# Kernel tuning notes

Hardware: AMD Instinct MI355X
Metric: run time of the kernel (lower is better)

Reference implementation:

```python
import jax, jax.numpy as jnp
import numpy as np

DIM = 768
NUM_HEADS = 8
HEAD_DIM = DIM // NUM_HEADS
SCALE = HEAD_DIM ** -0.5


def setup_inputs() -> dict:
    key = jax.random.key(0)
    k1, k2, k3, k4 = jax.random.split(key, 4)
    B, C, H, W = 8, DIM, 32, 32
    x = jax.random.normal(k1, (B, C, H, W), dtype=jnp.float32)
    # torch Linear stores weight as (out, in); y = x @ W.T + b
    w_qkv = jax.random.normal(k2, (3 * DIM, DIM), dtype=jnp.float32) * (DIM ** -0.5)
    w_proj = jax.random.normal(k3, (DIM, DIM), dtype=jnp.float32) * (DIM ** -0.5)
    b_proj = jax.random.normal(k4, (DIM,), dtype=jnp.float32) * 0.02
    return {"x": x, "w_qkv": w_qkv, "w_proj": w_proj, "b_proj": b_proj}


def reference(x, w_qkv, w_proj, b_proj):
    B, C, H, W = x.shape
    N = H * W
    nh, hd = NUM_HEADS, HEAD_DIM
    # (B, C, H, W) -> (B, N, C)
    tokens = x.reshape(B, C, N).transpose(0, 2, 1)
    qkv = tokens @ w_qkv.T  # (B, N, 3C), no bias (qkv_bias=False)
    qkv = qkv.reshape(B, N, 3, nh, hd).transpose(2, 0, 3, 1, 4)  # (3, B, nh, N, hd)
    q, k, v = qkv[0], qkv[1], qkv[2]
    attn = jnp.einsum('bhnd,bhmd->bhnm', q, k) * SCALE
    attn = jax.nn.softmax(attn, axis=-1)  # attn_drop=0.0 (eval)
    out = jnp.einsum('bhnm,bhmd->bhnd', attn, v)  # (B, nh, N, hd)
    out = out.transpose(0, 2, 1, 3).reshape(B, N, C)
    out = out @ w_proj.T + b_proj  # proj_drop=0.0
    return out.transpose(0, 2, 1).reshape(B, C, H, W)
```

## Files before the change

### kernel.cpp

```cpp
#include <hip/hip_runtime.h>

typedef short s16x8 __attribute__((ext_vector_type(8)));
typedef short s16x4 __attribute__((ext_vector_type(4)));
typedef float f32x4 __attribute__((ext_vector_type(4)));
typedef int   i32x4 __attribute__((ext_vector_type(4)));
typedef unsigned u32x2 __attribute__((ext_vector_type(2)));

#define SCALE_F 0.10206207261596577f
#define KLOG2E  0.14724444f
#define DEFER_THR 11.5415603f

__device__ __forceinline__ unsigned short f2bf(float f) {
  unsigned u = __builtin_bit_cast(unsigned, f);
  u += 0x7fffu + ((u >> 16) & 1u);
  return (unsigned short)(u >> 16);
}
__device__ __forceinline__ unsigned cvt_pk_bf16(float a, float b) {
  unsigned r;
  asm("v_cvt_pk_bf16_f32 %0, %1, %2" : "=v"(r) : "v"(a), "v"(b));
  return r;
}
__device__ __forceinline__ float exp2_fast(float x) {
  float r;
  asm("v_exp_f32 %0, %1" : "=v"(r) : "v"(x));
  return r;
}

#define MFMA16(a, b, c) __builtin_amdgcn_mfma_f32_16x16x32_bf16((a), (b), (c), 0, 0, 0)

__device__ __forceinline__ void gl_lds16(const unsigned short* g, unsigned short* l) {
  __builtin_amdgcn_global_load_lds(
      (const __attribute__((address_space(1))) void*)g,
      (__attribute__((address_space(3))) void*)l, 16, 0, 0);
}

__global__ __launch_bounds__(256) void cvt_bf16_kernel(const float* __restrict__ src,
                                                       unsigned short* __restrict__ dst, int n4) {
  int i = blockIdx.x * 256 + threadIdx.x;
  if (i >= n4) return;
  f32x4 v = reinterpret_cast<const f32x4*>(src)[i];
  s16x4 o;
  o[0] = (short)f2bf(v[0]); o[1] = (short)f2bf(v[1]);
  o[2] = (short)f2bf(v[2]); o[3] = (short)f2bf(v[3]);
  reinterpret_cast<s16x4*>(dst)[i] = o;
}

__global__ __launch_bounds__(256) void transpose_x_kernel(const float* __restrict__ x,
                                                          unsigned short* __restrict__ tokens) {
  __shared__ float t[32][33];
  const int ct = blockIdx.x * 32, nt = blockIdx.y * 32, b = blockIdx.z;
  const int tx = threadIdx.x, ty = threadIdx.y;
  const float* xp = x + (size_t)b * 768 * 1024;
#pragma unroll
  for (int r = 0; r < 4; ++r) {
    int c = ty + r * 8;
    t[c][tx] = xp[(size_t)(ct + c) * 1024 + nt + tx];
  }
  __syncthreads();
  unsigned short* tp = tokens + (size_t)b * 1024 * 768;
#pragma unroll
  for (int r = 0; r < 4; ++r) {
    int n = ty + r * 8;
    tp[(size_t)(nt + n) * 768 + ct + tx] = f2bf(t[tx][n]);
  }
}

__device__ __forceinline__ void stage128(const unsigned short* __restrict__ A,
                                         const unsigned short* __restrict__ Bt,
                                         unsigned short* lA, unsigned short* lB,
                                         int m0, int n0, int k0, int tid, int wave) {
  const int r2 = tid >> 2, s = tid & 3;
#pragma unroll
  for (int i = 0; i < 2; ++i) {
    const int row = i * 64 + r2;
    const int c = s ^ ((row >> 1) & 3);
    gl_lds16(A + (size_t)(m0 + row) * 768 + k0 + c * 8, lA + i * 2048 + wave * 512);
    gl_lds16(Bt + (size_t)(n0 + row) * 768 + k0 + c * 8, lB + i * 2048 + wave * 512);
  }
}

#define GEMM128_LOOP(A, Bt)                                                             \
  stage128(A, Bt, lA, lB, m0, n0, 0, tid, wave);                                        \
  __syncthreads();                                                                      \
  for (int t = 0; t < 24; ++t) {                                                        \
    const int cur = t & 1;                                                              \
    if (t < 23)                                                                         \
      stage128(A, Bt, lA + (cur ^ 1) * 4096, lB + (cur ^ 1) * 4096, m0, n0,             \
               (t + 1) * 32, tid, wave);                                                \
    s16x8 af[4], bf[4];                                                                 \
    _Pragma("unroll")                                                                   \
    for (int mi = 0; mi < 4; ++mi) {                                                    \
      const int row = wr * 64 + mi * 16 + lr;                                           \
      af[mi] = *reinterpret_cast<const s16x8*>(                                         \
          &lA[cur * 4096 + row * 32 + ((lg ^ ((row >> 1) & 3)) * 8)]);                  \
    }                                                                                   \
    _Pragma("unroll")                                                                   \
    for (int ni = 0; ni < 4; ++ni) {                                                    \
      const int row = wc * 64 + ni * 16 + lr;                                           \
      bf[ni] = *reinterpret_cast<const s16x8*>(                                         \
          &lB[cur * 4096 + row * 32 + ((lg ^ ((row >> 1) & 3)) * 8)]);                  \
    }                                                                                   \
    _Pragma("unroll")                                                                   \
    for (int mi = 0; mi < 4; ++mi)                                                      \
      _Pragma("unroll")                                                                 \
      for (int ni = 0; ni < 4; ++ni)                                                    \
        acc[mi][ni] = MFMA16(af[mi], bf[ni], acc[mi][ni]);                              \
    __syncthreads();                                                                    \
  }

__global__ __launch_bounds__(256, 4) void qkv_gemm_kernel(const unsigned short* __restrict__ A,
                                                          const unsigned short* __restrict__ Bt,
                                                          unsigned short* __restrict__ Qo,
                                                          unsigned short* __restrict__ Ko,
                                                          unsigned short* __restrict__ Vt) {
  __shared__ unsigned short lds_all[16384];
  unsigned short* lA = lds_all;
  unsigned short* lB = lds_all + 8192;

  const int tid = threadIdx.x;
  const int wave = tid >> 6, lane = tid & 63;
  const int wr = wave >> 1, wc = wave & 1;
  const int lr = lane & 15, lg = lane >> 4;
  const int bid = blockIdx.x;
  const int xcd = bid & 7, idx = bid >> 3;
  const int m0 = (xcd * 8 + idx / 18) * 128;
  const int n0 = (idx % 18) * 128;

  f32x4 acc[4][4] = {};
  GEMM128_LOOP(A, Bt)

  const int colbase = n0 + wc * 64;
  const int ttype = colbase / 768;
  if (ttype == 2) {
#pragma unroll
    for (int ni = 0; ni < 4; ++ni) {
      const int cc = colbase + ni * 16 + lr - 2 * 768;
      const int h = cc / 96, d = cc - h * 96;
#pragma unroll
      for (int mi = 0; mi < 4; ++mi) {
        const int gm = m0 + wr * 64 + mi * 16 + lg * 4;
        const int b = gm >> 10, n = gm & 1023;
        const int np = (n & ~31) | (((n >> 2) & 3) << 3) | (((n >> 4) & 1) << 2);
        u32x2 p2;
        p2[0] = cvt_pk_bf16(acc[mi][ni][0], acc[mi][ni][1]);
        p2[1] = cvt_pk_bf16(acc[mi][ni][2], acc[mi][ni][3]);
        *reinterpret_cast<s16x4*>(Vt + ((size_t)(b * 8 + h) * 96 + d) * 1024 + np) =
            __builtin_bit_cast(s16x4, p2);
      }
    }
  } else {
    unsigned short* W = lds_all + wave * 4096;
    unsigned short* dstbuf = (ttype == 0) ? Qo : Ko;
#pragma unroll
    for (int mi = 0; mi < 4; ++mi)
#pragma unroll
      for (int ni = 0; ni < 4; ++ni) {
        const int cc = ni * 16 + lr;
        const int ch = cc >> 3, wi = cc & 7;
#pragma unroll
        for (int j = 0; j < 4; ++j) {
          const int r = mi * 16 + lg * 4 + j;
          W[r * 64 + ((ch ^ (r & 7)) * 8) + wi] = f2bf(acc[mi][ni][j]);
        }
      }
    asm volatile("s_waitcnt lgkmcnt(0)" ::: "memory");
    __builtin_amdgcn_sched_barrier(0);
#pragma unroll
    for (int i = 0; i < 8; ++i) {
      const int r = i * 8 + (lane >> 3), c = lane & 7;
      s16x8 v8 = *reinterpret_cast<const s16x8*>(&W[r * 64 + ((c ^ (r & 7)) * 8)]);
      const int cc = colbase + c * 8 - ttype * 768;
      const int h = cc / 96, d = cc - h * 96;
      const int gm = m0 + wr * 64 + r;
      const int b = gm >> 10, n = gm & 1023;
      *reinterpret_cast<s16x8*>(dstbuf + ((size_t)(b * 8 + h) * 1024 + n) * 96 + d) = v8;
    }
  }
}

__global__ __launch_bounds__(256, 4) void proj_gemm_kernel(const unsigned short* __restrict__ A,
                                                           const unsigned short* __restrict__ Bt,
                                                           const float* __restrict__ bias,
                                                           float* __restrict__ out) {
  __shared__ unsigned short lds_all[16384];
  unsigned short* lA = lds_all;
  unsigned short* lB = lds_all + 8192;

  const int tid = threadIdx.x;
  const int wave = tid >> 6, lane = tid & 63;
  const int wr = wave >> 1, wc = wave & 1;
  const int lr = lane & 15, lg = lane >> 4;
  const int bid = blockIdx.x;
  const int xcd = bid & 7, idx = bid >> 3;
  const int m0 = (xcd * 8 + idx / 6) * 128;
  const int n0 = (idx % 6) * 128;

  f32x4 acc[4][4] = {};
  GEMM128_LOOP(A, Bt)

#pragma unroll
  for (int ni = 0; ni < 4; ++ni) {
    const int col = n0 + wc * 64 + ni * 16 + lr;
    const float bv = bias[col];
#pragma unroll
    for (int mi = 0; mi < 4; ++mi) {
      const int gm = m0 + wr * 64 + mi * 16 + lg * 4;
      const int b = gm >> 10, n = gm & 1023;
      f32x4 v;
#pragma unroll
      for (int j = 0; j < 4; ++j) v[j] = acc[mi][ni][j] + bv;
      *reinterpret_cast<f32x4*>(out + (size_t)b * 768 * 1024 + (size_t)col * 1024 + n) = v;
    }
  }
}

__global__ __launch_bounds__(512, 4) void attn_kernel(const unsigned short* __restrict__ Q,
                                                      const unsigned short* __restrict__ K,
                                                      const unsigned short* __restrict__ Vt,
                                                      unsigned short* __restrict__ Ao) {
  __shared__ unsigned short lds[2][12288];

  const int f = blockIdx.x;
  const int xcd = f & 7;
  const int g = (f >> 3) + xcd * 64;
  const int bh = g >> 3, qb = g & 7;

  const int tid = threadIdx.x, wave = tid >> 6, lane = tid & 63;
  const int lr = lane & 15, lg = lane >> 4;
  const int klo = (lr >> 1) & 3;

  const unsigned short* Qp = Q + (size_t)bh * 1024 * 96;
  const unsigned short* Kp = K + (size_t)bh * 1024 * 96;
  const unsigned short* Vp = Vt + (size_t)bh * 96 * 1024;

  const int qrow = qb * 128 + wave * 16 + lr;
  s16x8 qreg[3];
#pragma unroll
  for (int kd = 0; kd < 3; ++kd)
    qreg[kd] = *reinterpret_cast<const s16x8*>(Qp + (size_t)qrow * 96 + kd * 32 + lg * 8);

  float m2 = -1e30f, l_r = 0.f;
  f32x4 oacc[6] = {};

#define STAGE(bufi, kv0)                                                              \
  {                                                                                   \
    _Pragma("unroll")                                                                 \
    for (int i = 0; i < 3; ++i) {                                                     \
      const int wl = wave + 8 * i;                                                    \
      if (wl < 12) {                                                                  \
        const int kd = wl >> 2, rg = wl & 3;                                          \
        const int row = rg * 16 + (lane >> 2);                                        \
        const int c8 = (lane & 3) ^ ((row >> 1) & 3);                                 \
        gl_lds16(Kp + (size_t)((kv0) + row) * 96 + kd * 32 + c8 * 8,                  \
                 &lds[bufi][0] + kd * 2048 + rg * 512);                               \
      } else {                                                                        \
        const int v = wl - 12;                                                        \
        const int gs = v / 6, rg = v - gs * 6;                                        \
        const int drow = rg * 16 + (lane >> 2);                                       \
        const int c8 = (lane & 3) ^ ((drow >> 1) & 3);                                \
        gl_lds16(Vp + (size_t)drow * 1024 + (kv0) + gs * 32 + c8 * 8,                 \
                 &lds[bufi][0] + 6144 + gs * 3072 + rg * 512);                        \
      }                                                                               \
    }                                                                                 \
  }

  STAGE(0, 0);
  __syncthreads();

  for (int gt = 0; gt < 16; ++gt) {
    const int buf = gt & 1;
    if (gt < 15) STAGE(buf ^ 1, (gt + 1) * 64);

    f32x4 sacc[4] = {};
    __builtin_amdgcn_s_setprio(1);
#pragma unroll
    for (int c = 0; c < 4; ++c) {
#pragma unroll
      for (int kd = 0; kd < 3; ++kd) {
        s16x8 kf = *reinterpret_cast<const s16x8*>(
            &lds[buf][kd * 2048 + (c * 16 + lr) * 32 + ((lg ^ klo) * 8)]);
        sacc[c] = MFMA16(kf, qreg[kd], sacc[c]);
      }
    }
    __builtin_amdgcn_s_setprio(0);

    float mx = fmaxf(fmaxf(sacc[0][0], sacc[0][1]), fmaxf(sacc[0][2], sacc[0][3]));
#pragma unroll
    for (int c = 1; c < 4; ++c)
      mx = fmaxf(mx, fmaxf(fmaxf(sacc[c][0], sacc[c][1]), fmaxf(sacc[c][2], sacc[c][3])));
    mx = fmaxf(mx, __shfl_xor(mx, 16));
    mx = fmaxf(mx, __shfl_xor(mx, 32));
    const float mc = mx * KLOG2E;
    if (!__all(mc - m2 <= DEFER_THR)) {
      const float m2n = fmaxf(m2, mc);
      const float rsc = exp2_fast(m2 - m2n);
      l_r *= rsc;
#pragma unroll
      for (int dt = 0; dt < 6; ++dt) oacc[dt] *= rsc;
      m2 = m2n;
    }
    float ts = 0.f;
    unsigned pk[4][2];
#pragma unroll
    for (int c = 0; c < 4; ++c) {
      float p0 = exp2_fast(__builtin_fmaf(sacc[c][0], KLOG2E, -m2));
      float p1 = exp2_fast(__builtin_fmaf(sacc[c][1], KLOG2E, -m2));
      float p2 = exp2_fast(__builtin_fmaf(sacc[c][2], KLOG2E, -m2));
      float p3 = exp2_fast(__builtin_fmaf(sacc[c][3], KLOG2E, -m2));
      ts += (p0 + p1) + (p2 + p3);
      pk[c][0] = cvt_pk_bf16(p0, p1);
      pk[c][1] = cvt_pk_bf16(p2, p3);
    }
    ts += __shfl_xor(ts, 16);
    ts += __shfl_xor(ts, 32);
    l_r += ts;

    __builtin_amdgcn_s_setprio(1);
#pragma unroll
    for (int gs = 0; gs < 2; ++gs) {
      i32x4 bi;
      bi[0] = (int)pk[2 * gs][0];
      bi[1] = (int)pk[2 * gs][1];
      bi[2] = (int)pk[2 * gs + 1][0];
      bi[3] = (int)pk[2 * gs + 1][1];
      s16x8 pf = __builtin_bit_cast(s16x8, bi);
#pragma unroll
      for (int dt = 0; dt < 6; ++dt) {
        s16x8 vf = *reinterpret_cast<const s16x8*>(
            &lds[buf][6144 + gs * 3072 + (dt * 16 + lr) * 32 + ((lg ^ klo) * 8)]);
        oacc[dt] = MFMA16(vf, pf, oacc[dt]);
      }
    }
    __builtin_amdgcn_s_setprio(0);
    __syncthreads();
  }

  const float invl = 1.0f / l_r;
  const int b_ = bh >> 3, h_ = bh & 7;
  unsigned short* orow = Ao + (size_t)(b_ * 1024 + qrow) * 768 + h_ * 96;
#pragma unroll
  for (int dt = 0; dt < 6; ++dt) {
    u32x2 p2;
    p2[0] = cvt_pk_bf16(oacc[dt][0] * invl, oacc[dt][1] * invl);
    p2[1] = cvt_pk_bf16(oacc[dt][2] * invl, oacc[dt][3] * invl);
    *reinterpret_cast<s16x4*>(orow + dt * 16 + lg * 4) = __builtin_bit_cast(s16x4, p2);
  }
#undef STAGE
}

extern "C" void kernel_launch(void* const* d_in, const int* in_sizes, int n_in,
                              void* d_out, int out_size, void* d_ws, size_t ws_size,
                              hipStream_t stream) {
  const float* x = (const float*)d_in[0];
  const float* wqkv = (const float*)d_in[1];
  const float* wproj = (const float*)d_in[2];
  const float* bproj = (const float*)d_in[3];
  float* out = (float*)d_out;

  unsigned short* ws = (unsigned short*)d_ws;
  unsigned short* tokens = ws;
  unsigned short* wqkv_b = tokens + 8192 * 768;
  unsigned short* wproj_b = wqkv_b + 2304 * 768;
  unsigned short* Qb = wproj_b + 768 * 768;
  unsigned short* Kb = Qb + 64 * 1024 * 96;
  unsigned short* Vb = Kb + 64 * 1024 * 96;
  unsigned short* Ab = Vb + 64 * 1024 * 96;

  cvt_bf16_kernel<<<1728, 256, 0, stream>>>(wqkv, wqkv_b, 2304 * 768 / 4);
  cvt_bf16_kernel<<<576, 256, 0, stream>>>(wproj, wproj_b, 768 * 768 / 4);
  transpose_x_kernel<<<dim3(24, 32, 8), dim3(32, 8), 0, stream>>>(x, tokens);
  qkv_gemm_kernel<<<1152, 256, 0, stream>>>(tokens, wqkv_b, Qb, Kb, Vb);
  attn_kernel<<<512, 512, 0, stream>>>(Qb, Kb, Vb, Ab);
  proj_gemm_kernel<<<384, 256, 0, stream>>>(Ab, wproj_b, bproj, out);
}
```

Baseline: 119.1 us.

## Rewrite QKV GEMM with 256x128 tiles and triple-buffered async LDS pipeline

The QKV projection GEMM now uses 512-thread blocks computing 256x128 output tiles, so each block shares one staged B tile across twice as many rows. It also uses a three-stage LDS ring with direct global-to-LDS loads issued two k-steps ahead, explicit vmcnt waits and s_setprio around the MFMA block. The aim is to hide global load latency and cut B-operand traffic. In exchange it uses larger LDS per block and launches half as many blocks, which may lower occupancy, and the hand-placed waits and barriers have to be exactly right.

```diff
diff --git a/kernel.cpp b/kernel.cpp
--- a/kernel.cpp
+++ b/kernel.cpp
@@ -62,6 +62,136 @@
   for (int r = 0; r < 4; ++r) {
     int n = ty + r * 8;
     tp[(size_t)(nt + n) * 768 + ct + tx] = f2bf(t[tx][n]);
+  }
+}
+
+__global__ __launch_bounds__(512, 4) void qkv_gemm_kernel(const unsigned short* __restrict__ A,
+                                                          const unsigned short* __restrict__ Bt,
+                                                          unsigned short* __restrict__ Qo,
+                                                          unsigned short* __restrict__ Ko,
+                                                          unsigned short* __restrict__ Vt) {
+  __shared__ unsigned short lds[36864];
+  const int tid = threadIdx.x;
+  const int wave = tid >> 6, lane = tid & 63;
+  const int wm = wave >> 1, wn = wave & 1;
+  const int lr = lane & 15, lg = lane >> 4;
+  const int bid = blockIdx.x;
+  const int xcd = bid & 7, idx = bid >> 3;
+  const int m0 = (xcd * 4 + idx / 18) * 256;
+  const int n0 = (idx % 18) * 128;
+
+  const int srow = tid >> 2, sslot = tid & 3;
+
+  f32x4 acc[4][4] = {};
+
+#define STAGE_KT(ktv, bb)                                                       \
+  {                                                                             \
+    unsigned short* lb = lds + (bb) * 12288;                                    \
+    _Pragma("unroll")                                                           \
+    for (int rr = 0; rr < 2; ++rr) {                                            \
+      const int row = rr * 128 + srow;                                          \
+      const int c = sslot ^ ((row >> 1) & 3);                                   \
+      gl_lds16(A + (size_t)(m0 + row) * 768 + (ktv) * 32 + c * 8,               \
+               lb + rr * 4096 + wave * 512);                                    \
+    }                                                                           \
+    {                                                                           \
+      const int c = sslot ^ ((srow >> 1) & 3);                                  \
+      gl_lds16(Bt + (size_t)(n0 + srow) * 768 + (ktv) * 32 + c * 8,             \
+               lb + 8192 + wave * 512);                                         \
+    }                                                                           \
+  }
+
+  STAGE_KT(0, 0)
+  STAGE_KT(1, 1)
+  asm volatile("s_waitcnt vmcnt(3)" ::: "memory");
+  __builtin_amdgcn_s_barrier();
+
+  int cb = 0;
+  for (int kt = 0; kt < 24; ++kt) {
+    unsigned short* curb = lds + cb * 12288;
+    s16x8 af[4], bf[4];
+#pragma unroll
+    for (int mi = 0; mi < 4; ++mi) {
+      const int row = wm * 64 + mi * 16 + lr;
+      af[mi] = *reinterpret_cast<const s16x8*>(
+          &curb[row * 32 + ((lg ^ ((row >> 1) & 3)) * 8)]);
+    }
+#pragma unroll
+    for (int ni = 0; ni < 4; ++ni) {
+      const int row = wn * 64 + ni * 16 + lr;
+      bf[ni] = *reinterpret_cast<const s16x8*>(
+          &curb[8192 + row * 32 + ((lg ^ ((row >> 1) & 3)) * 8)]);
+    }
+    if (kt < 22) {
+      const int sb = (cb == 0) ? 2 : cb - 1;
+      STAGE_KT(kt + 2, sb)
+    }
+    __builtin_amdgcn_s_barrier();
+    asm volatile("s_waitcnt lgkmcnt(0)" ::: "memory");
+    __builtin_amdgcn_sched_barrier(0);
+    __builtin_amdgcn_s_setprio(1);
+#pragma unroll
+    for (int mi = 0; mi < 4; ++mi)
+#pragma unroll
+      for (int ni = 0; ni < 4; ++ni)
+        acc[mi][ni] = MFMA16(af[mi], bf[ni], acc[mi][ni]);
+    __builtin_amdgcn_s_setprio(0);
+    if (kt < 22) {
+      asm volatile("s_waitcnt vmcnt(3)" ::: "memory");
+    } else if (kt == 22) {
+      asm volatile("s_waitcnt vmcnt(0)" ::: "memory");
+    }
+    __builtin_amdgcn_s_barrier();
+    cb = (cb == 2) ? 0 : cb + 1;
+  }
+#undef STAGE_KT
+
+  const int colbase = n0 + wn * 64;
+  const int ttype = colbase / 768;
+  if (ttype == 2) {
+#pragma unroll
+    for (int ni = 0; ni < 4; ++ni) {
+      const int cc = colbase + ni * 16 + lr - 2 * 768;
+      const int h = cc / 96, d = cc - h * 96;
+#pragma unroll
+      for (int mi = 0; mi < 4; ++mi) {
+        const int gm = m0 + wm * 64 + mi * 16 + lg * 4;
+        const int b = gm >> 10, n = gm & 1023;
+        const int np = (n & ~31) | (((n >> 2) & 3) << 3) | (((n >> 4) & 1) << 2);
+        u32x2 p2;
+        p2[0] = cvt_pk_bf16(acc[mi][ni][0], acc[mi][ni][1]);
+        p2[1] = cvt_pk_bf16(acc[mi][ni][2], acc[mi][ni][3]);
+        *reinterpret_cast<s16x4*>(Vt + ((size_t)(b * 8 + h) * 96 + d) * 1024 + np) =
+            __builtin_bit_cast(s16x4, p2);
+      }
+    }
+  } else {
+    unsigned short* W = lds + wave * 4096;
+    unsigned short* dstbuf = (ttype == 0) ? Qo : Ko;
+#pragma unroll
+    for (int mi = 0; mi < 4; ++mi)
+#pragma unroll
+      for (int ni = 0; ni < 4; ++ni) {
+        const int cc = ni * 16 + lr;
+        const int ch = cc >> 3, wi = cc & 7;
+#pragma unroll
+        for (int j = 0; j < 4; ++j) {
+          const int r = mi * 16 + lg * 4 + j;
+          W[r * 64 + ((ch ^ (r & 7)) * 8) + wi] = f2bf(acc[mi][ni][j]);
+        }
+      }
+    asm volatile("s_waitcnt lgkmcnt(0)" ::: "memory");
+    __builtin_amdgcn_sched_barrier(0);
+#pragma unroll
+    for (int i = 0; i < 8; ++i) {
+      const int r = i * 8 + (lane >> 3), c = lane & 7;
+      s16x8 v8 = *reinterpret_cast<const s16x8*>(&W[r * 64 + ((c ^ (r & 7)) * 8)]);
+      const int cc = colbase + c * 8 - ttype * 768;
+      const int h = cc / 96, d = cc - h * 96;
+      const int gm = m0 + wm * 64 + r;
+      const int b = gm >> 10, n = gm & 1023;
+      *reinterpret_cast<s16x8*>(dstbuf + ((size_t)(b * 8 + h) * 1024 + n) * 96 + d) = v8;
+    }
   }
 }
 
@@ -108,76 +238,6 @@
     __syncthreads();                                                                    \
   }
 
-__global__ __launch_bounds__(256, 4) void qkv_gemm_kernel(const unsigned short* __restrict__ A,
-                                                          const unsigned short* __restrict__ Bt,
-                                                          unsigned short* __restrict__ Qo,
-                                                          unsigned short* __restrict__ Ko,
-                                                          unsigned short* __restrict__ Vt) {
-  __shared__ unsigned short lds_all[16384];
-  unsigned short* lA = lds_all;
-  unsigned short* lB = lds_all + 8192;
-
-  const int tid = threadIdx.x;
-  const int wave = tid >> 6, lane = tid & 63;
-  const int wr = wave >> 1, wc = wave & 1;
-  const int lr = lane & 15, lg = lane >> 4;
-  const int bid = blockIdx.x;
-  const int xcd = bid & 7, idx = bid >> 3;
-  const int m0 = (xcd * 8 + idx / 18) * 128;
-  const int n0 = (idx % 18) * 128;
-
-  f32x4 acc[4][4] = {};
-  GEMM128_LOOP(A, Bt)
-
-  const int colbase = n0 + wc * 64;
-  const int ttype = colbase / 768;
-  if (ttype == 2) {
-#pragma unroll
-    for (int ni = 0; ni < 4; ++ni) {
-      const int cc = colbase + ni * 16 + lr - 2 * 768;
-      const int h = cc / 96, d = cc - h * 96;
-#pragma unroll
-      for (int mi = 0; mi < 4; ++mi) {
-        const int gm = m0 + wr * 64 + mi * 16 + lg * 4;
-        const int b = gm >> 10, n = gm & 1023;
-        const int np = (n & ~31) | (((n >> 2) & 3) << 3) | (((n >> 4) & 1) << 2);
-        u32x2 p2;
-        p2[0] = cvt_pk_bf16(acc[mi][ni][0], acc[mi][ni][1]);
-        p2[1] = cvt_pk_bf16(acc[mi][ni][2], acc[mi][ni][3]);
-        *reinterpret_cast<s16x4*>(Vt + ((size_t)(b * 8 + h) * 96 + d) * 1024 + np) =
-            __builtin_bit_cast(s16x4, p2);
-      }
-    }
-  } else {
-    unsigned short* W = lds_all + wave * 4096;
-    unsigned short* dstbuf = (ttype == 0) ? Qo : Ko;
-#pragma unroll
-    for (int mi = 0; mi < 4; ++mi)
-#pragma unroll
-      for (int ni = 0; ni < 4; ++ni) {
-        const int cc = ni * 16 + lr;
-        const int ch = cc >> 3, wi = cc & 7;
-#pragma unroll
-        for (int j = 0; j < 4; ++j) {
-          const int r = mi * 16 + lg * 4 + j;
-          W[r * 64 + ((ch ^ (r & 7)) * 8) + wi] = f2bf(acc[mi][ni][j]);
-        }
-      }
-    asm volatile("s_waitcnt lgkmcnt(0)" ::: "memory");
-    __builtin_amdgcn_sched_barrier(0);
-#pragma unroll
-    for (int i = 0; i < 8; ++i) {
-      const int r = i * 8 + (lane >> 3), c = lane & 7;
-      s16x8 v8 = *reinterpret_cast<const s16x8*>(&W[r * 64 + ((c ^ (r & 7)) * 8)]);
-      const int cc = colbase + c * 8 - ttype * 768;
-      const int h = cc / 96, d = cc - h * 96;
-      const int gm = m0 + wr * 64 + r;
-      const int b = gm >> 10, n = gm & 1023;
-      *reinterpret_cast<s16x8*>(dstbuf + ((size_t)(b * 8 + h) * 1024 + n) * 96 + d) = v8;
-    }
-  }
-}
-
 __global__ __launch_bounds__(256, 4) void proj_gemm_kernel(const unsigned short* __restrict__ A,
                                                            const unsigned short* __restrict__ Bt,
                                                            const float* __restrict__ bias,
@@ -369,7 +429,7 @@
   cvt_bf16_kernel<<<1728, 256, 0, stream>>>(wqkv, wqkv_b, 2304 * 768 / 4);
   cvt_bf16_kernel<<<576, 256, 0, stream>>>(wproj, wproj_b, 768 * 768 / 4);
   transpose_x_kernel<<<dim3(24, 32, 8), dim3(32, 8), 0, stream>>>(x, tokens);
-  qkv_gemm_kernel<<<1152, 256, 0, stream>>>(tokens, wqkv_b, Qb, Kb, Vb);
+  qkv_gemm_kernel<<<576, 512, 0, stream>>>(tokens, wqkv_b, Qb, Kb, Vb);
   attn_kernel<<<512, 512, 0, stream>>>(Qb, Kb, Vb, Ab);
   proj_gemm_kernel<<<384, 256, 0, stream>>>(Ab, wproj_b, bproj, out);
 }
```

New measurement: 116.7 us. 1.02x faster.

## Register-staged prefetch pipeline for GEMMs and 256-row QKV tiles with 8 waves

Applied to the files above, without the earlier changes.

Both GEMM kernels drop the direct global-to-LDS staging and instead load two k-steps ahead into registers, then write them to the alternate LDS buffer after the MFMAs, with setprio around the MFMA block. The QKV GEMM also moves to 512-thread blocks covering 256x128 tiles, so each block loads the B tile once for twice the rows, halving the grid. This trades extra VGPRs and lower occupancy for deeper prefetch and more reuse of B. The epilogue LDS scratch now indexes per wave across 8 waves (32K shorts), which fits.

```diff
diff --git a/kernel.cpp b/kernel.cpp
--- a/kernel.cpp
+++ b/kernel.cpp
@@ -65,71 +65,85 @@
   }
 }
 
-__device__ __forceinline__ void stage128(const unsigned short* __restrict__ A,
-                                         const unsigned short* __restrict__ Bt,
-                                         unsigned short* lA, unsigned short* lB,
-                                         int m0, int n0, int k0, int tid, int wave) {
-  const int r2 = tid >> 2, s = tid & 3;
-#pragma unroll
-  for (int i = 0; i < 2; ++i) {
-    const int row = i * 64 + r2;
-    const int c = s ^ ((row >> 1) & 3);
-    gl_lds16(A + (size_t)(m0 + row) * 768 + k0 + c * 8, lA + i * 2048 + wave * 512);
-    gl_lds16(Bt + (size_t)(n0 + row) * 768 + k0 + c * 8, lB + i * 2048 + wave * 512);
-  }
-}
-
-#define GEMM128_LOOP(A, Bt)                                                             \
-  stage128(A, Bt, lA, lB, m0, n0, 0, tid, wave);                                        \
-  __syncthreads();                                                                      \
-  for (int t = 0; t < 24; ++t) {                                                        \
-    const int cur = t & 1;                                                              \
-    if (t < 23)                                                                         \
-      stage128(A, Bt, lA + (cur ^ 1) * 4096, lB + (cur ^ 1) * 4096, m0, n0,             \
-               (t + 1) * 32, tid, wave);                                                \
-    s16x8 af[4], bf[4];                                                                 \
-    _Pragma("unroll")                                                                   \
-    for (int mi = 0; mi < 4; ++mi) {                                                    \
-      const int row = wr * 64 + mi * 16 + lr;                                           \
-      af[mi] = *reinterpret_cast<const s16x8*>(                                         \
-          &lA[cur * 4096 + row * 32 + ((lg ^ ((row >> 1) & 3)) * 8)]);                  \
-    }                                                                                   \
-    _Pragma("unroll")                                                                   \
-    for (int ni = 0; ni < 4; ++ni) {                                                    \
-      const int row = wc * 64 + ni * 16 + lr;                                           \
-      bf[ni] = *reinterpret_cast<const s16x8*>(                                         \
-          &lB[cur * 4096 + row * 32 + ((lg ^ ((row >> 1) & 3)) * 8)]);                  \
-    }                                                                                   \
-    _Pragma("unroll")                                                                   \
-    for (int mi = 0; mi < 4; ++mi)                                                      \
-      _Pragma("unroll")                                                                 \
-      for (int ni = 0; ni < 4; ++ni)                                                    \
-        acc[mi][ni] = MFMA16(af[mi], bf[ni], acc[mi][ni]);                              \
-    __syncthreads();                                                                    \
-  }
-
-__global__ __launch_bounds__(256, 4) void qkv_gemm_kernel(const unsigned short* __restrict__ A,
+__global__ __launch_bounds__(512, 2) void qkv_gemm_kernel(const unsigned short* __restrict__ A,
                                                           const unsigned short* __restrict__ Bt,
                                                           unsigned short* __restrict__ Qo,
                                                           unsigned short* __restrict__ Ko,
                                                           unsigned short* __restrict__ Vt) {
-  __shared__ unsigned short lds_all[16384];
-  unsigned short* lA = lds_all;
-  unsigned short* lB = lds_all + 8192;
-
+  __shared__ __align__(16) unsigned short lds[32768];
   const int tid = threadIdx.x;
   const int wave = tid >> 6, lane = tid & 63;
-  const int wr = wave >> 1, wc = wave & 1;
+  const int wm = wave >> 1, wn = wave & 1;
   const int lr = lane & 15, lg = lane >> 4;
   const int bid = blockIdx.x;
   const int xcd = bid & 7, idx = bid >> 3;
-  const int m0 = (xcd * 8 + idx / 18) * 128;
+  const int m0 = (xcd * 4 + idx / 18) * 256;
   const int n0 = (idx % 18) * 128;
 
+  const int ar0 = tid >> 2, ar1 = (tid + 512) >> 2, ac = tid & 3;
+  const unsigned short* pA0 = A + (size_t)(m0 + ar0) * 768 + ac * 8;
+  const unsigned short* pA1 = A + (size_t)(m0 + ar1) * 768 + ac * 8;
+  const unsigned short* pB = Bt + (size_t)(n0 + ar0) * 768 + ac * 8;
+  const int offA0 = ar0 * 32 + ((ac ^ ((ar0 >> 1) & 3)) * 8);
+  const int offA1 = ar1 * 32 + ((ac ^ ((ar1 >> 1) & 3)) * 8);
+  const int offB = 8192 + ar0 * 32 + ((ac ^ ((ar0 >> 1) & 3)) * 8);
+
   f32x4 acc[4][4] = {};
-  GEMM128_LOOP(A, Bt)
-
-  const int colbase = n0 + wc * 64;
+  i32x4 s0a0, s0a1, s0b, s1a0, s1a1, s1b;
+
+#define LOADG(kt, ra0, ra1, rb)                                               \
+  ra0 = *reinterpret_cast<const i32x4*>(pA0 + (size_t)(kt) * 32);             \
+  ra1 = *reinterpret_cast<const i32x4*>(pA1 + (size_t)(kt) * 32);             \
+  rb = *reinterpret_cast<const i32x4*>(pB + (size_t)(kt) * 32);
+
+#define WRITELDS(bi, ra0, ra1, rb)                                            \
+  {                                                                           \
+    unsigned short* wb = lds + (bi) * 12288;                                  \
+    *reinterpret_cast<i32x4*>(wb + offA0) = ra0;                              \
+    *reinterpret_cast<i32x4*>(wb + offA1) = ra1;                              \
+    *reinterpret_cast<i32x4*>(wb + offB) = rb;                                \
+  }
+
+#define QKV_ITER(kt, la0, la1, lb, wa0, wa1, wb_)                             \
+  {                                                                           \
+    const unsigned short* cb = lds + ((kt)&1) * 12288;                        \
+    s16x8 af[4], bf[4];                                                       \
+    _Pragma("unroll") for (int mi = 0; mi < 4; ++mi) {                        \
+      const int row = wm * 64 + mi * 16 + lr;                                 \
+      af[mi] = *reinterpret_cast<const s16x8*>(                               \
+          &cb[row * 32 + ((lg ^ ((row >> 1) & 3)) * 8)]);                     \
+    }                                                                         \
+    _Pragma("unroll") for (int ni = 0; ni < 4; ++ni) {                        \
+      const int row = wn * 64 + ni * 16 + lr;                                 \
+      bf[ni] = *reinterpret_cast<const s16x8*>(                               \
+          &cb[8192 + row * 32 + ((lg ^ ((row >> 1) & 3)) * 8)]);              \
+    }                                                                         \
+    if ((kt) < 22) { LOADG((kt) + 2, la0, la1, lb) }                          \
+    __builtin_amdgcn_s_setprio(1);                                            \
+    _Pragma("unroll") for (int mi = 0; mi < 4; ++mi)                          \
+        _Pragma("unroll") for (int ni = 0; ni < 4; ++ni)                      \
+            acc[mi][ni] = MFMA16(af[mi], bf[ni], acc[mi][ni]);                \
+    __builtin_amdgcn_s_setprio(0);                                            \
+    if ((kt) < 23) { WRITELDS(((kt) + 1) & 1, wa0, wa1, wb_) }                \
+    asm volatile("s_waitcnt lgkmcnt(0)" ::: "memory");                        \
+    __builtin_amdgcn_s_barrier();                                             \
+  }
+
+  LOADG(0, s0a0, s0a1, s0b)
+  LOADG(1, s1a0, s1a1, s1b)
+  WRITELDS(0, s0a0, s0a1, s0b)
+  asm volatile("s_waitcnt lgkmcnt(0)" ::: "memory");
+  __builtin_amdgcn_s_barrier();
+
+  for (int kt2 = 0; kt2 < 24; kt2 += 2) {
+    QKV_ITER(kt2, s0a0, s0a1, s0b, s1a0, s1a1, s1b)
+    QKV_ITER(kt2 + 1, s1a0, s1a1, s1b, s0a0, s0a1, s0b)
+  }
+#undef QKV_ITER
+#undef LOADG
+#undef WRITELDS
+
+  const int colbase = n0 + wn * 64;
   const int ttype = colbase / 768;
   if (ttype == 2) {
 #pragma unroll
@@ -138,7 +152,7 @@
       const int h = cc / 96, d = cc - h * 96;
 #pragma unroll
       for (int mi = 0; mi < 4; ++mi) {
-        const int gm = m0 + wr * 64 + mi * 16 + lg * 4;
+        const int gm = m0 + wm * 64 + mi * 16 + lg * 4;
         const int b = gm >> 10, n = gm & 1023;
         const int np = (n & ~31) | (((n >> 2) & 3) << 3) | (((n >> 4) & 1) << 2);
         u32x2 p2;
@@ -149,7 +163,7 @@
       }
     }
   } else {
-    unsigned short* W = lds_all + wave * 4096;
+    unsigned short* W = lds + wave * 4096;
     unsigned short* dstbuf = (ttype == 0) ? Qo : Ko;
 #pragma unroll
     for (int mi = 0; mi < 4; ++mi)
@@ -171,7 +185,7 @@
       s16x8 v8 = *reinterpret_cast<const s16x8*>(&W[r * 64 + ((c ^ (r & 7)) * 8)]);
       const int cc = colbase + c * 8 - ttype * 768;
       const int h = cc / 96, d = cc - h * 96;
-      const int gm = m0 + wr * 64 + r;
+      const int gm = m0 + wm * 64 + r;
       const int b = gm >> 10, n = gm & 1023;
       *reinterpret_cast<s16x8*>(dstbuf + ((size_t)(b * 8 + h) * 1024 + n) * 96 + d) = v8;
     }
@@ -182,10 +196,7 @@
                                                            const unsigned short* __restrict__ Bt,
                                                            const float* __restrict__ bias,
                                                            float* __restrict__ out) {
-  __shared__ unsigned short lds_all[16384];
-  unsigned short* lA = lds_all;
-  unsigned short* lB = lds_all + 8192;
-
+  __shared__ __align__(16) unsigned short lds[16384];
   const int tid = threadIdx.x;
   const int wave = tid >> 6, lane = tid & 63;
   const int wr = wave >> 1, wc = wave & 1;
@@ -195,8 +206,70 @@
   const int m0 = (xcd * 8 + idx / 6) * 128;
   const int n0 = (idx % 6) * 128;
 
+  const int r0 = tid >> 2, r1 = (tid + 256) >> 2, ac = tid & 3;
+  const unsigned short* pA0 = A + (size_t)(m0 + r0) * 768 + ac * 8;
+  const unsigned short* pA1 = A + (size_t)(m0 + r1) * 768 + ac * 8;
+  const unsigned short* pB0 = Bt + (size_t)(n0 + r0) * 768 + ac * 8;
+  const unsigned short* pB1 = Bt + (size_t)(n0 + r1) * 768 + ac * 8;
+  const int off0 = r0 * 32 + ((ac ^ ((r0 >> 1) & 3)) * 8);
+  const int off1 = r1 * 32 + ((ac ^ ((r1 >> 1) & 3)) * 8);
+
   f32x4 acc[4][4] = {};
-  GEMM128_LOOP(A, Bt)
+  i32x4 s0a0, s0a1, s0b0, s0b1, s1a0, s1a1, s1b0, s1b1;
+
+#define LOADG(kt, ra0, ra1, rb0, rb1)                                         \
+  ra0 = *reinterpret_cast<const i32x4*>(pA0 + (size_t)(kt) * 32);             \
+  ra1 = *reinterpret_cast<const i32x4*>(pA1 + (size_t)(kt) * 32);             \
+  rb0 = *reinterpret_cast<const i32x4*>(pB0 + (size_t)(kt) * 32);             \
+  rb1 = *reinterpret_cast<const i32x4*>(pB1 + (size_t)(kt) * 32);
+
+#define WRITELDS(bi, ra0, ra1, rb0, rb1)                                      \
+  {                                                                           \
+    unsigned short* wb = lds + (bi) * 8192;                                   \
+    *reinterpret_cast<i32x4*>(wb + off0) = ra0;                               \
+    *reinterpret_cast<i32x4*>(wb + off1) = ra1;                               \
+    *reinterpret_cast<i32x4*>(wb + 4096 + off0) = rb0;                        \
+    *reinterpret_cast<i32x4*>(wb + 4096 + off1) = rb1;                        \
+  }
+
+#define PROJ_ITER(kt, la0, la1, lb0, lb1, wa0, wa1, wb0, wb1)                 \
+  {                                                                           \
+    const unsigned short* cb = lds + ((kt)&1) * 8192;                         \
+    s16x8 af[4], bf[4];                                                       \
+    _Pragma("unroll") for (int mi = 0; mi < 4; ++mi) {                        \
+      const int row = wr * 64 + mi * 16 + lr;                                 \
+      af[mi] = *reinterpret_cast<const s16x8*>(                               \
+          &cb[row * 32 + ((lg ^ ((row >> 1) & 3)) * 8)]);                     \
+    }                                                                         \
+    _Pragma("unroll") for (int ni = 0; ni < 4; ++ni) {                        \
+      const int row = wc * 64 + ni * 16 + lr;                                 \
+      bf[ni] = *reinterpret_cast<const s16x8*>(                               \
+          &cb[4096 + row * 32 + ((lg ^ ((row >> 1) & 3)) * 8)]);              \
+    }                                                                         \
+    if ((kt) < 22) { LOADG((kt) + 2, la0, la1, lb0, lb1) }                    \
+    __builtin_amdgcn_s_setprio(1);                                            \
+    _Pragma("unroll") for (int mi = 0; mi < 4; ++mi)                          \
+        _Pragma("unroll") for (int ni = 0; ni < 4; ++ni)                      \
+            acc[mi][ni] = MFMA16(af[mi], bf[ni], acc[mi][ni]);                \
+    __builtin_amdgcn_s_setprio(0);                                            \
+    if ((kt) < 23) { WRITELDS(((kt) + 1) & 1, wa0, wa1, wb0, wb1) }           \
+    asm volatile("s_waitcnt lgkmcnt(0)" ::: "memory");                        \
+    __builtin_amdgcn_s_barrier();                                             \
+  }
+
+  LOADG(0, s0a0, s0a1, s0b0, s0b1)
+  LOADG(1, s1a0, s1a1, s1b0, s1b1)
+  WRITELDS(0, s0a0, s0a1, s0b0, s0b1)
+  asm volatile("s_waitcnt lgkmcnt(0)" ::: "memory");
+  __builtin_amdgcn_s_barrier();
+
+  for (int kt2 = 0; kt2 < 24; kt2 += 2) {
+    PROJ_ITER(kt2, s0a0, s0a1, s0b0, s0b1, s1a0, s1a1, s1b0, s1b1)
+    PROJ_ITER(kt2 + 1, s1a0, s1a1, s1b0, s1b1, s0a0, s0a1, s0b0, s0b1)
+  }
+#undef PROJ_ITER
+#undef LOADG
+#undef WRITELDS
 
 #pragma unroll
   for (int ni = 0; ni < 4; ++ni) {
@@ -369,7 +442,7 @@
   cvt_bf16_kernel<<<1728, 256, 0, stream>>>(wqkv, wqkv_b, 2304 * 768 / 4);
   cvt_bf16_kernel<<<576, 256, 0, stream>>>(wproj, wproj_b, 768 * 768 / 4);
   transpose_x_kernel<<<dim3(24, 32, 8), dim3(32, 8), 0, stream>>>(x, tokens);
-  qkv_gemm_kernel<<<1152, 256, 0, stream>>>(tokens, wqkv_b, Qb, Kb, Vb);
+  qkv_gemm_kernel<<<576, 512, 0, stream>>>(tokens, wqkv_b, Qb, Kb, Vb);
   attn_kernel<<<512, 512, 0, stream>>>(Qb, Kb, Vb, Ab);
   proj_gemm_kernel<<<384, 256, 0, stream>>>(Ab, wproj_b, bproj, out);
 }
```

Measured after the change: 156.6 us. 31.5% more time.
